# Kernel optimization log

Hardware: AMD Instinct MI355X
Metric: run time of the kernel (lower is better)

Reference implementation:

```python
import jax, jax.numpy as jnp
import numpy as np

N = 100000
E = 1600000
F_IN = 256   # 4 * 64 after concat
H = 128

def _glorot(key, shape):
    fan_in, fan_out = shape
    lim = jnp.sqrt(6.0 / (fan_in + fan_out))
    return jax.random.uniform(key, shape, jnp.float32, -lim, lim)

def setup_inputs() -> dict:
    key = jax.random.key(0)
    ks = jax.random.split(key, 32)
    inp = {
        'x': jax.random.normal(ks[0], (N, 64), jnp.float32),
        'diff': jax.random.normal(ks[1], (N, 64), jnp.float32),
        'rec_prev': jax.random.normal(ks[2], (N, 64), jnp.float32),
        'hidden_prev': jax.random.normal(ks[3], (N, 64), jnp.float32),
        'edge_index': jax.random.randint(ks[4], (2, E), 0, N, jnp.int64),
    }
    dims = [(F_IN, H), (H, H), (H, H), (H, 1)]
    for i, (din, dout) in enumerate(dims):
        inp[f'Wl{i}'] = _glorot(ks[5 + 3 * i], (din, dout))  # neighbor (aggr) weight
        inp[f'Wr{i}'] = _glorot(ks[6 + 3 * i], (din, dout))  # root weight
        inp[f'b{i}'] = jnp.zeros((dout,), jnp.float32)
    return inp

def _sage_conv(h, src, dst, Wl, Wr, b):
    # mean aggregation of source-node features at destination nodes (PyG SAGEConv)
    msg_sum = jax.ops.segment_sum(h[src], dst, num_segments=N)        # [N, F]
    cnt = jax.ops.segment_sum(jnp.ones((src.shape[0],), h.dtype), dst, num_segments=N)
    mean = msg_sum / jnp.maximum(cnt, 1.0)[:, None]
    return mean @ Wl + h @ Wr + b

def reference(x, diff, rec_prev, hidden_prev, edge_index,
              Wl0, Wr0, b0, Wl1, Wr1, b1, Wl2, Wr2, b2, Wl3, Wr3, b3):
    src, dst = edge_index[0], edge_index[1]
    h = jnp.concatenate([x, diff, rec_prev, hidden_prev], axis=1)  # [N, 256]
    params = [(Wl0, Wr0, b0), (Wl1, Wr1, b1), (Wl2, Wr2, b2), (Wl3, Wr3, b3)]
    h = _sage_conv(h, src, dst, *params[0])
    for Wl, Wr, b in params[1:]:
        h = jax.nn.relu(h)
        h = _sage_conv(h, src, dst, Wl, Wr, b)
    out = jax.nn.sigmoid(h)          # [N, 1]
    lwp_util = jnp.mean(out)
    return out, lwp_util
```

## Files before the change

### kernel.cpp

```cpp
#include <hip/hip_runtime.h>
#include <hip/hip_bf16.h>

#define NN 100000
#define EE 1600000
#define HH 128
#define NB 391
#define CAP 5120
#define GB 1563
#define SB 64
#define EPB (EE / SB)

typedef short bf16x8 __attribute__((ext_vector_type(8)));
typedef short bf16x4 __attribute__((ext_vector_type(4)));
typedef float f32x4  __attribute__((ext_vector_type(4)));

__device__ inline short f2bf(float v) {
    __hip_bfloat16 b = __float2bfloat16(v);
    return *reinterpret_cast<short*>(&b);
}

typedef __attribute__((address_space(1))) void gvoid_t;
typedef __attribute__((address_space(3))) void svoid_t;
__device__ __forceinline__ void gload16(const void* g, void* l) {
    __builtin_amdgcn_global_load_lds((gvoid_t*)g, (svoid_t*)l, 16, 0, 0);
}

__device__ __forceinline__ void ld_fence() { asm volatile("" ::: "memory"); }

template <int N>
__device__ __forceinline__ void wait_vm_bar() {
    if constexpr (N == 0)
        asm volatile("s_waitcnt vmcnt(0)\n\ts_barrier" ::: "memory");
    else if constexpr (N == 8)
        asm volatile("s_waitcnt vmcnt(8)\n\ts_barrier" ::: "memory");
    else if constexpr (N == 12)
        asm volatile("s_waitcnt vmcnt(12)\n\ts_barrier" ::: "memory");
    else if constexpr (N == 16)
        asm volatile("s_waitcnt vmcnt(16)\n\ts_barrier" ::: "memory");
    else if constexpr (N == 18)
        asm volatile("s_waitcnt vmcnt(18)\n\ts_barrier" ::: "memory");
    else if constexpr (N == 20)
        asm volatile("s_waitcnt vmcnt(20)\n\ts_barrier" ::: "memory");
    else
        static_assert(N == 0 || N == 8 || N == 12 || N == 16 || N == 18 || N == 20,
                      "bad N");
}
__device__ __forceinline__ void barrier_only() {
    asm volatile("s_barrier" ::: "memory");
}

__global__ __launch_bounds__(1024) void prep_kernel(
    const float* __restrict__ Wl0, const float* __restrict__ Wr0,
    const float* __restrict__ Wl1, const float* __restrict__ Wr1,
    const float* __restrict__ Wl2, const float* __restrict__ Wr2,
    __hip_bfloat16* __restrict__ WT0, __hip_bfloat16* __restrict__ WT1,
    __hip_bfloat16* __restrict__ WT2, int* __restrict__ bcur) {
    const int t = threadIdx.x;
    if (blockIdx.x == 128) {
        if (t < NB) bcur[t] = 0;
        return;
    }
    int id = blockIdx.x * 1024 + t;
    if (id < 65536) {
        int k = id & 255, n = id >> 8;
        float v = (n < 128) ? Wl0[(size_t)k * 128 + n]
                            : Wr0[(size_t)k * 128 + (n - 128)];
        WT0[(size_t)n * 256 + k] = __float2bfloat16(v);
    } else {
        id -= 65536;
        int layer = id >> 15;
        int u = id & 32767;
        int k = u & 127, n = u >> 7;
        const float* Wl = layer ? Wl2 : Wl1;
        const float* Wr = layer ? Wr2 : Wr1;
        __hip_bfloat16* WT = layer ? WT2 : WT1;
        float v = (n < 128) ? Wl[(size_t)k * 128 + n]
                            : Wr[(size_t)k * 128 + (n - 128)];
        WT[(size_t)n * 128 + k] = __float2bfloat16(v);
    }
}

#define EW 264
template <int K, bool FIRST>
__device__ __forceinline__ void gemm_body(
    short* __restrict__ lsh, int bid,
    const __hip_bfloat16* hin,
    const float* __restrict__ x0, const float* __restrict__ x1,
    const float* __restrict__ x2, const float* __restrict__ x3,
    const __hip_bfloat16* __restrict__ wt, const float* __restrict__ bias,
    __hip_bfloat16* zout, __hip_bfloat16* __restrict__ rout) {
    const int t    = threadIdx.x;
    const int w    = t >> 6;
    const int lane = t & 63;
    const int quad = lane >> 4;
    const int l16  = lane & 15;
    const int n0   = bid * 64;

    constexpr int BUFB = FIRST ? 16384 : 8192;
    char* const lc = (char*)lsh;

    const __hip_bfloat16* afeat[4];
#pragma unroll
    for (int ft = 0; ft < 4; ++ft)
        afeat[ft] = wt + (size_t)(w * 64 + ft * 16 + l16) * K + quad * 8;

    f32x4 acc[4][4];
#pragma unroll
    for (int ft = 0; ft < 4; ++ft)
#pragma unroll
        for (int nt = 0; nt < 4; ++nt)
            acc[ft][nt] = (f32x4){0.f, 0.f, 0.f, 0.f};

    bf16x8 wreg[2][8];

    auto loadW = [&](int p, int pb) {
#pragma unroll
        for (int kcl = 0; kcl < 2; ++kcl)
#pragma unroll
            for (int ft = 0; ft < 4; ++ft)
                wreg[pb][kcl * 4 + ft] =
                    *(const bf16x8*)(afeat[ft] + (p * 2 + kcl) * 32);
    };

    auto stage = [&](int p, int bb) {
        char* lb = lc + bb * BUFB;
        if constexpr (FIRST) {
            const float* sp = (p == 0) ? x0 : (p == 1) ? x1 : (p == 2) ? x2 : x3;
#pragma unroll
            for (int i = 0; i < 4; ++i) {
                const int j   = w * 4 + i;
                const int row = j * 4 + (lane >> 4);
                int rg = n0 + row; if (rg > NN - 1) rg = NN - 1;
                const int colb = ((lane & 15) * 16) ^ ((row & 15) << 4);
                gload16((const char*)sp + (size_t)rg * 256 + colb, lb + j * 1024);
            }
        } else {
#pragma unroll
            for (int i = 0; i < 2; ++i) {
                const int j   = w * 2 + i;
                const int row = j * 8 + (lane >> 3);
                int rg = n0 + row; if (rg > NN - 1) rg = NN - 1;
                const int colb = ((lane & 7) * 16) ^ ((row & 7) << 4);
                gload16((const char*)hin + (size_t)rg * 256 + p * 128 + colb,
                        lb + j * 1024);
            }
        }
    };

    auto compute = [&](int s, int bb, int pb) {
        const char* lb = lc + (bb)*BUFB;
#pragma unroll
        for (int kcl = 0; kcl < 2; ++kcl) {
#pragma unroll
            for (int nt = 0; nt < 4; ++nt) {
                const int row = nt * 16 + l16;
                bf16x8 b;
                if constexpr (FIRST) {
                    const int sw = (row & 15) << 4;
                    const int B0 = kcl * 128 + quad * 32;
                    const char* rb = lb + row * 256;
                    const f32x4 lo = *(const f32x4*)(rb + ((B0) ^ sw));
                    const f32x4 hi = *(const f32x4*)(rb + ((B0 + 16) ^ sw));
                    b[0] = f2bf(lo[0]); b[1] = f2bf(lo[1]);
                    b[2] = f2bf(lo[2]); b[3] = f2bf(lo[3]);
                    b[4] = f2bf(hi[0]); b[5] = f2bf(hi[1]);
                    b[6] = f2bf(hi[2]); b[7] = f2bf(hi[3]);
                } else {
                    const int sw = (row & 7) << 4;
                    const int B0 = kcl * 64 + quad * 16;
                    b = *(const bf16x8*)(lb + row * 128 + (B0 ^ sw));
                }
#pragma unroll
                for (int ft = 0; ft < 4; ++ft)
                    acc[ft][nt] = __builtin_amdgcn_mfma_f32_16x16x32_bf16(
                        wreg[pb][kcl * 4 + ft], b, acc[ft][nt], 0, 0, 0);
            }
        }
    };

    if constexpr (FIRST) {
        stage(0, 0); ld_fence();
        stage(1, 1); ld_fence();
        loadW(0, 0); ld_fence();
        wait_vm_bar<12>(); loadW(1, 1); stage(2, 2); compute(0, 0, 0); barrier_only();
        wait_vm_bar<20>(); loadW(2, 0); stage(3, 0); compute(1, 1, 1); barrier_only();
        wait_vm_bar<12>(); loadW(3, 1);              compute(2, 2, 0); barrier_only();
        wait_vm_bar<8>();                            compute(3, 0, 1); barrier_only();
    } else {
        stage(0, 0); ld_fence();
        stage(1, 1); ld_fence();
        loadW(0, 0); loadW(1, 1);
        wait_vm_bar<18>(); compute(0, 0, 0); barrier_only();
        wait_vm_bar<16>(); compute(1, 1, 1); barrier_only();
    }

#pragma unroll
    for (int ft = 0; ft < 4; ++ft) {
        const int fb = ft * 16 + quad * 4;
        float4 bv = make_float4(0.f, 0.f, 0.f, 0.f);
        if (w >= 2) bv = *(const float4*)&bias[(w - 2) * 64 + fb];
        const int cbase = (w & 1) * 64 + ((w >= 2) ? 128 : 0);
#pragma unroll
        for (int nt = 0; nt < 4; ++nt) {
            const f32x4 a = acc[ft][nt];
            bf16x4 p;
            p[0] = f2bf(a[0] + bv.x); p[1] = f2bf(a[1] + bv.y);
            p[2] = f2bf(a[2] + bv.z); p[3] = f2bf(a[3] + bv.w);
            *(bf16x4*)&lsh[(nt * 16 + l16) * EW + cbase + fb] = p;
        }
    }
    __syncthreads();
#pragma unroll
    for (int u = 0; u < 8; ++u) {
        const int id  = u * 256 + t;
        const int row = id >> 5, ch = (id & 31) * 8;
        const int nd  = n0 + row;
        if (nd < NN) {
            const bf16x8 v = *(const bf16x8*)&lsh[row * EW + ch];
            if (ch < 128) *(bf16x8*)&zout[(size_t)nd * HH + ch] = v;
            else          *(bf16x8*)&rout[(size_t)nd * HH + (ch - 128)] = v;
        }
    }
}

template <int K, bool FIRST>
__global__ __launch_bounds__(256) void gemm_kernel(
    const __hip_bfloat16* hin,
    const float* __restrict__ x0, const float* __restrict__ x1,
    const float* __restrict__ x2, const float* __restrict__ x3,
    const __hip_bfloat16* __restrict__ wt, const float* __restrict__ bias,
    __hip_bfloat16* zout, __hip_bfloat16* __restrict__ rout) {
    __shared__ short lsh[16896];
    gemm_body<K, FIRST>(lsh, blockIdx.x, hin, x0, x1, x2, x3, wt, bias, zout, rout);
}

__global__ __launch_bounds__(256) void gemm0_scatter_kernel(
    const float* __restrict__ x0, const float* __restrict__ x1,
    const float* __restrict__ x2, const float* __restrict__ x3,
    const __hip_bfloat16* __restrict__ wt, const float* __restrict__ bias,
    __hip_bfloat16* __restrict__ zout, __hip_bfloat16* __restrict__ rout,
    const int* __restrict__ srcv, const int* __restrict__ dstv,
    int* __restrict__ bcur, int* __restrict__ pairs) {
    __shared__ short lsh[24576];
    const int t = threadIdx.x;

    if (blockIdx.x >= SB) {
        gemm_body<256, true>(lsh, blockIdx.x - SB, nullptr, x0, x1, x2, x3,
                             wt, bias, zout, rout);
        return;
    }

    int* hist = (int*)lsh;
    int* base = hist + NB;
    for (int j = t; j < NB; j += 256) hist[j] = 0;
    __syncthreads();

    const int e0   = blockIdx.x * EPB;
    const int eend_ = e0 + EPB;

    for (int be = e0; be < eend_; be += 4096) {
        int d[16];
#pragma unroll
        for (int u = 0; u < 16; ++u) {
            const int e = be + u * 256 + t;
            d[u] = (e < eend_) ? dstv[e] : -1;
        }
#pragma unroll
        for (int u = 0; u < 16; ++u)
            if (d[u] >= 0) atomicAdd(&hist[d[u] >> 8], 1);
    }
    __syncthreads();

    for (int j = t; j < NB; j += 256)
        base[j] = hist[j] ? atomicAdd(&bcur[j], hist[j]) : 0;
    __syncthreads();
    for (int j = t; j < NB; j += 256) hist[j] = base[j];
    __syncthreads();

    for (int be = e0; be < eend_; be += 4096) {
        int s[16], d[16];
#pragma unroll
        for (int u = 0; u < 16; ++u) {
            const int e = be + u * 256 + t;
            if (e < eend_) { s[u] = srcv[e]; d[u] = dstv[e]; }
            else d[u] = -1;
        }
#pragma unroll
        for (int u = 0; u < 16; ++u)
            if (d[u] >= 0) {
                const int b   = d[u] >> 8;
                const int pos = atomicAdd(&hist[b], 1);
                if (pos < CAP) pairs[b * CAP + pos] = (s[u] << 8) | (d[u] & 255);
            }
    }
}

__global__ __launch_bounds__(256) void finalize_kernel(
    const int* __restrict__ bcur, const int* __restrict__ pairs,
    int* __restrict__ csr, int* __restrict__ beg, int* __restrict__ eend,
    float* __restrict__ inv) {
    __shared__ int cnt[256];
    __shared__ int scn[256];
    __shared__ int cur[256];
    const int b = blockIdx.x, t = threadIdx.x;
    int m = bcur[b];
    if (m > CAP) m = CAP;

    cnt[t] = 0;
    __syncthreads();
    for (int e = t; e < m; e += 256)
        atomicAdd(&cnt[pairs[b * CAP + e] & 255], 1);
    __syncthreads();

    const int v = cnt[t];
    scn[t] = v;
    __syncthreads();
    for (int st = 1; st < 256; st <<= 1) {
        int tv = (t >= st) ? scn[t - st] : 0;
        __syncthreads();
        scn[t] += tv;
        __syncthreads();
    }
    const int myStart = scn[t] - v;
    cur[t] = myStart;
    __syncthreads();

    for (int e = t; e < m; e += 256) {
        const int pk  = pairs[b * CAP + e];
        const int pos = atomicAdd(&cur[pk & 255], 1);
        csr[b * CAP + pos] = pk >> 8;
    }

    const int node = b * 256 + t;
    if (node < NN) {
        beg[node]  = b * CAP + myStart;
        eend[node] = b * CAP + myStart + v;
        inv[node]  = 1.0f / fmaxf((float)v, 1.0f);
    }
}

template <bool LAST>
__global__ __launch_bounds__(256) void aggregate_kernel(
    const __hip_bfloat16* __restrict__ z, __hip_bfloat16* __restrict__ rio,
    const int* __restrict__ beg, const int* __restrict__ eend,
    const int* __restrict__ csr, const float* __restrict__ inv,
    const float* __restrict__ Wl3, const float* __restrict__ Wr3,
    const float* __restrict__ b3, float* __restrict__ z3,
    float* __restrict__ r3) {
    const int i    = (blockIdx.x * 256 + threadIdx.x) >> 6;
    const int lane = threadIdx.x & 63;
    const int g    = lane >> 4;
    const int l16  = lane & 15;
    if (i >= NN) return;
    const int b0 = beg[i], e0 = eend[i];

    float acc[8];
#pragma unroll
    for (int j = 0; j < 8; ++j) acc[j] = 0.f;

    int e = b0 + g;
    for (; e + 12 < e0; e += 16) {
        const int s0 = csr[e];
        const int s1 = csr[e + 4];
        const int s2 = csr[e + 8];
        const int s3 = csr[e + 12];
        const bf16x8 z0 = *(const bf16x8*)&z[(size_t)s0 * HH + l16 * 8];
        const bf16x8 z1 = *(const bf16x8*)&z[(size_t)s1 * HH + l16 * 8];
        const bf16x8 z2 = *(const bf16x8*)&z[(size_t)s2 * HH + l16 * 8];
        const bf16x8 z3v = *(const bf16x8*)&z[(size_t)s3 * HH + l16 * 8];
        const __hip_bfloat162* p0 = (const __hip_bfloat162*)&z0;
        const __hip_bfloat162* p1 = (const __hip_bfloat162*)&z1;
        const __hip_bfloat162* p2 = (const __hip_bfloat162*)&z2;
        const __hip_bfloat162* p3 = (const __hip_bfloat162*)&z3v;
#pragma unroll
        for (int j = 0; j < 4; ++j) {
            acc[2 * j]     += __bfloat162float(p0[j].x) + __bfloat162float(p1[j].x)
                            + __bfloat162float(p2[j].x) + __bfloat162float(p3[j].x);
            acc[2 * j + 1] += __bfloat162float(p0[j].y) + __bfloat162float(p1[j].y)
                            + __bfloat162float(p2[j].y) + __bfloat162float(p3[j].y);
        }
    }
    for (; e < e0; e += 4) {
        const int s0 = csr[e];
        const bf16x8 z0 = *(const bf16x8*)&z[(size_t)s0 * HH + l16 * 8];
        const __hip_bfloat162* p0 = (const __hip_bfloat162*)&z0;
#pragma unroll
        for (int j = 0; j < 4; ++j) {
            acc[2 * j]     += __bfloat162float(p0[j].x);
            acc[2 * j + 1] += __bfloat162float(p0[j].y);
        }
    }

#pragma unroll
    for (int j = 0; j < 8; ++j) {
        acc[j] += __shfl_xor(acc[j], 16, 64);
        acc[j] += __shfl_xor(acc[j], 32, 64);
    }

    const float iv = inv[i];
    const int   f  = l16 * 8 + g * 2;
    const __hip_bfloat162 rv = *(const __hip_bfloat162*)&rio[(size_t)i * HH + f];
    const float ox = fmaxf(acc[g * 2]     * iv + __bfloat162float(rv.x), 0.f);
    const float oy = fmaxf(acc[g * 2 + 1] * iv + __bfloat162float(rv.y), 0.f);

    if (!LAST) {
        __hip_bfloat162 o;
        o.x = __float2bfloat16(ox);
        o.y = __float2bfloat16(oy);
        *(__hip_bfloat162*)&rio[(size_t)i * HH + f] = o;
    } else {
        const float2 wl = *(const float2*)&Wl3[f];
        const float2 wr = *(const float2*)&Wr3[f];
        float al = ox * wl.x + oy * wl.y;
        float ar = ox * wr.x + oy * wr.y;
#pragma unroll
        for (int m = 32; m; m >>= 1) {
            al += __shfl_xor(al, m, 64);
            ar += __shfl_xor(ar, m, 64);
        }
        if (lane == 0) {
            z3[i] = al;
            r3[i] = ar + b3[0];
        }
    }
}

__global__ __launch_bounds__(256) void final_kernel(
    const float* __restrict__ z3, const float* __restrict__ r3,
    const int* __restrict__ beg, const int* __restrict__ eend,
    const int* __restrict__ csr, const float* __restrict__ inv,
    float* __restrict__ out, float* __restrict__ partial) {
    __shared__ float red[4];
    const int i    = (blockIdx.x * 256 + threadIdx.x) >> 6;
    const int lane = threadIdx.x & 63;
    const int w    = threadIdx.x >> 6;
    float v = 0.f;
    if (i < NN) {
        const int b0 = beg[i], e0 = eend[i];
        float a = 0.f;
        for (int e = b0 + lane; e < e0; e += 64) a += z3[csr[e]];
#pragma unroll
        for (int m = 32; m; m >>= 1) a += __shfl_xor(a, m, 64);
        const float pre = a * inv[i] + r3[i];
        const float s = 1.f / (1.f + __expf(-pre));
        if (lane == 0) { out[i] = s; v = s; }
    }
    if (lane == 0) red[w] = v;
    __syncthreads();
    if (threadIdx.x == 0)
        partial[blockIdx.x] = red[0] + red[1] + red[2] + red[3];
}

__global__ __launch_bounds__(256) void mean_kernel(const float* __restrict__ partial,
                                                   int nb, float* __restrict__ out) {
    __shared__ float lds[256];
    float s = 0.f;
    for (int i = threadIdx.x; i < nb; i += 256) s += partial[i];
    lds[threadIdx.x] = s;
    __syncthreads();
    for (int st = 128; st; st >>= 1) {
        if (threadIdx.x < st) lds[threadIdx.x] += lds[threadIdx.x + st];
        __syncthreads();
    }
    if (threadIdx.x == 0) out[NN] = lds[0] / (float)NN;
}

extern "C" void kernel_launch(void* const* d_in, const int* in_sizes, int n_in,
                              void* d_out, int out_size, void* d_ws, size_t ws_size,
                              hipStream_t stream) {
    const float* x    = (const float*)d_in[0];
    const float* diff = (const float*)d_in[1];
    const float* rec  = (const float*)d_in[2];
    const float* hid  = (const float*)d_in[3];
    const int* edge   = (const int*)d_in[4];
    const int* esrc = edge;
    const int* edst = edge + EE;
    const float* Wl0 = (const float*)d_in[5];
    const float* Wr0 = (const float*)d_in[6];
    const float* b0  = (const float*)d_in[7];
    const float* Wl1 = (const float*)d_in[8];
    const float* Wr1 = (const float*)d_in[9];
    const float* b1  = (const float*)d_in[10];
    const float* Wl2 = (const float*)d_in[11];
    const float* Wr2 = (const float*)d_in[12];
    const float* b2  = (const float*)d_in[13];
    const float* Wl3 = (const float*)d_in[14];
    const float* Wr3 = (const float*)d_in[15];
    const float* b3  = (const float*)d_in[16];
    float* out = (float*)d_out;

    char* w = (char*)d_ws;
    auto alloc = [&](size_t bytes) -> void* {
        void* p = (void*)w;
        w += (bytes + 255) & ~(size_t)255;
        return p;
    };
    __hip_bfloat16* bufA = (__hip_bfloat16*)alloc((size_t)NN * HH * 2);
    __hip_bfloat16* bufB = (__hip_bfloat16*)alloc((size_t)NN * HH * 2);
    __hip_bfloat16* WT0  = (__hip_bfloat16*)alloc((size_t)256 * 256 * 2);
    __hip_bfloat16* WT1  = (__hip_bfloat16*)alloc((size_t)256 * 128 * 2);
    __hip_bfloat16* WT2  = (__hip_bfloat16*)alloc((size_t)256 * 128 * 2);
    int*   pairs   = (int*)alloc((size_t)NB * CAP * 4);
    int*   csr     = (int*)alloc((size_t)NB * CAP * 4);
    int*   bcur    = (int*)alloc((size_t)512 * 4);
    int*   beg     = (int*)alloc((size_t)NN * 4);
    int*   eend    = (int*)alloc((size_t)NN * 4);
    float* inv     = (float*)alloc((size_t)NN * 4);
    float* z3      = (float*)alloc((size_t)NN * 4);
    float* r3      = (float*)alloc((size_t)NN * 4);
    float* partial = (float*)alloc((size_t)25000 * 4);

    const int WB = (NN + 3) / 4;

    prep_kernel<<<129, 1024, 0, stream>>>(Wl0, Wr0, Wl1, Wr1, Wl2, Wr2,
                                          WT0, WT1, WT2, bcur);

    gemm0_scatter_kernel<<<GB + SB, 256, 0, stream>>>(
        x, diff, rec, hid, WT0, b0, bufA, bufB, esrc, edst, bcur, pairs);

    finalize_kernel<<<NB, 256, 0, stream>>>(bcur, pairs, csr, beg, eend, inv);

    aggregate_kernel<false><<<WB, 256, 0, stream>>>(bufA, bufB, beg, eend, csr, inv,
                                                    nullptr, nullptr, nullptr,
                                                    nullptr, nullptr);

    gemm_kernel<128, false><<<GB, 256, 0, stream>>>(bufB, nullptr, nullptr, nullptr, nullptr,
                                                    WT1, b1, bufB, bufA);
    aggregate_kernel<false><<<WB, 256, 0, stream>>>(bufB, bufA, beg, eend, csr, inv,
                                                    nullptr, nullptr, nullptr,
                                                    nullptr, nullptr);

    gemm_kernel<128, false><<<GB, 256, 0, stream>>>(bufA, nullptr, nullptr, nullptr, nullptr,
                                                    WT2, b2, bufA, bufB);
    aggregate_kernel<true><<<WB, 256, 0, stream>>>(bufA, bufB, beg, eend, csr, inv,
                                                   Wl3, Wr3, b3, z3, r3);

    final_kernel<<<WB, 256, 0, stream>>>(z3, r3, beg, eend, csr, inv, out, partial);
    mean_kernel<<<1, 256, 0, stream>>>(partial, WB, out);
}
```

Measured before the change: 497.7 us.

## Split fused gemm0/scatter kernel and issue all GEMM tile loads upfront

Separates the combined first-layer GEMM plus edge-scatter kernel into a standalone scatter kernel (now 256 blocks instead of 64) and a dedicated gemm0 kernel. The GEMM body no longer double-buffers: it loads all weight fragments and stages all K-slices into LDS at once (larger LDS, 64KB for the first layer), then waits on decreasing vmcnt thresholds and computes each slice as it arrives. The aim is more memory parallelism per block and more scatter parallelism. The cost is an extra kernel launch and the loss of concurrent scatter/GEMM overlap. Higher register and LDS use may also lower occupancy.

```diff
diff --git a/kernel.cpp b/kernel.cpp
--- a/kernel.cpp
+++ b/kernel.cpp
@@ -7,7 +7,7 @@
 #define NB 391
 #define CAP 5120
 #define GB 1563
-#define SB 64
+#define SB 256
 #define EPB (EE / SB)
 
 typedef short bf16x8 __attribute__((ext_vector_type(8)));
@@ -31,19 +31,16 @@
 __device__ __forceinline__ void wait_vm_bar() {
     if constexpr (N == 0)
         asm volatile("s_waitcnt vmcnt(0)\n\ts_barrier" ::: "memory");
+    else if constexpr (N == 2)
+        asm volatile("s_waitcnt vmcnt(2)\n\ts_barrier" ::: "memory");
+    else if constexpr (N == 4)
+        asm volatile("s_waitcnt vmcnt(4)\n\ts_barrier" ::: "memory");
     else if constexpr (N == 8)
         asm volatile("s_waitcnt vmcnt(8)\n\ts_barrier" ::: "memory");
     else if constexpr (N == 12)
         asm volatile("s_waitcnt vmcnt(12)\n\ts_barrier" ::: "memory");
-    else if constexpr (N == 16)
-        asm volatile("s_waitcnt vmcnt(16)\n\ts_barrier" ::: "memory");
-    else if constexpr (N == 18)
-        asm volatile("s_waitcnt vmcnt(18)\n\ts_barrier" ::: "memory");
-    else if constexpr (N == 20)
-        asm volatile("s_waitcnt vmcnt(20)\n\ts_barrier" ::: "memory");
     else
-        static_assert(N == 0 || N == 8 || N == 12 || N == 16 || N == 18 || N == 20,
-                      "bad N");
+        static_assert(N == 0 || N == 2 || N == 4 || N == 8 || N == 12, "bad N");
 }
 __device__ __forceinline__ void barrier_only() {
     asm volatile("s_barrier" ::: "memory");
@@ -96,6 +93,7 @@
     const int l16  = lane & 15;
     const int n0   = bid * 64;
 
+    constexpr int NS   = K / 64;
     constexpr int BUFB = FIRST ? 16384 : 8192;
     char* const lc = (char*)lsh;
 
@@ -111,19 +109,19 @@
         for (int nt = 0; nt < 4; ++nt)
             acc[ft][nt] = (f32x4){0.f, 0.f, 0.f, 0.f};
 
-    bf16x8 wreg[2][8];
-
-    auto loadW = [&](int p, int pb) {
+    bf16x8 wreg[NS][8];
+
+    auto loadW = [&](int p) {
 #pragma unroll
         for (int kcl = 0; kcl < 2; ++kcl)
 #pragma unroll
             for (int ft = 0; ft < 4; ++ft)
-                wreg[pb][kcl * 4 + ft] =
+                wreg[p][kcl * 4 + ft] =
                     *(const bf16x8*)(afeat[ft] + (p * 2 + kcl) * 32);
     };
 
-    auto stage = [&](int p, int bb) {
-        char* lb = lc + bb * BUFB;
+    auto stage = [&](int p) {
+        char* lb = lc + p * BUFB;
         if constexpr (FIRST) {
             const float* sp = (p == 0) ? x0 : (p == 1) ? x1 : (p == 2) ? x2 : x3;
 #pragma unroll
@@ -147,8 +145,8 @@
         }
     };
 
-    auto compute = [&](int s, int bb, int pb) {
-        const char* lb = lc + (bb)*BUFB;
+    auto compute = [&](int s) {
+        const char* lb = lc + s * BUFB;
 #pragma unroll
         for (int kcl = 0; kcl < 2; ++kcl) {
 #pragma unroll
@@ -173,25 +171,29 @@
 #pragma unroll
                 for (int ft = 0; ft < 4; ++ft)
                     acc[ft][nt] = __builtin_amdgcn_mfma_f32_16x16x32_bf16(
-                        wreg[pb][kcl * 4 + ft], b, acc[ft][nt], 0, 0, 0);
+                        wreg[s][kcl * 4 + ft], b, acc[ft][nt], 0, 0, 0);
             }
         }
     };
 
     if constexpr (FIRST) {
-        stage(0, 0); ld_fence();
-        stage(1, 1); ld_fence();
-        loadW(0, 0); ld_fence();
-        wait_vm_bar<12>(); loadW(1, 1); stage(2, 2); compute(0, 0, 0); barrier_only();
-        wait_vm_bar<20>(); loadW(2, 0); stage(3, 0); compute(1, 1, 1); barrier_only();
-        wait_vm_bar<12>(); loadW(3, 1);              compute(2, 2, 0); barrier_only();
-        wait_vm_bar<8>();                            compute(3, 0, 1); barrier_only();
+        loadW(0); loadW(1); loadW(2); loadW(3); ld_fence();
+        stage(0); ld_fence();
+        stage(1); ld_fence();
+        stage(2); ld_fence();
+        stage(3); ld_fence();
+        wait_vm_bar<12>(); compute(0);
+        wait_vm_bar<8>();  compute(1);
+        wait_vm_bar<4>();  compute(2);
+        wait_vm_bar<0>();  compute(3);
+        barrier_only();
     } else {
-        stage(0, 0); ld_fence();
-        stage(1, 1); ld_fence();
-        loadW(0, 0); loadW(1, 1);
-        wait_vm_bar<18>(); compute(0, 0, 0); barrier_only();
-        wait_vm_bar<16>(); compute(1, 1, 1); barrier_only();
+        loadW(0); loadW(1); ld_fence();
+        stage(0); ld_fence();
+        stage(1); ld_fence();
+        wait_vm_bar<2>(); compute(0);
+        wait_vm_bar<0>(); compute(1);
+        barrier_only();
     }
 
 #pragma unroll
@@ -223,39 +225,37 @@
     }
 }
 
-template <int K, bool FIRST>
-__global__ __launch_bounds__(256) void gemm_kernel(
-    const __hip_bfloat16* hin,
+__global__ __launch_bounds__(256, 2) void gemm0_kernel(
     const float* __restrict__ x0, const float* __restrict__ x1,
     const float* __restrict__ x2, const float* __restrict__ x3,
     const __hip_bfloat16* __restrict__ wt, const float* __restrict__ bias,
+    __hip_bfloat16* __restrict__ zout, __hip_bfloat16* __restrict__ rout) {
+    __shared__ short lsh[32768];
+    gemm_body<256, true>(lsh, blockIdx.x, nullptr, x0, x1, x2, x3,
+                         wt, bias, zout, rout);
+}
+
+template <int K>
+__global__ __launch_bounds__(256) void gemm_kernel(
+    const __hip_bfloat16* hin,
+    const __hip_bfloat16* __restrict__ wt, const float* __restrict__ bias,
     __hip_bfloat16* zout, __hip_bfloat16* __restrict__ rout) {
     __shared__ short lsh[16896];
-    gemm_body<K, FIRST>(lsh, blockIdx.x, hin, x0, x1, x2, x3, wt, bias, zout, rout);
-}
-
-__global__ __launch_bounds__(256) void gemm0_scatter_kernel(
-    const float* __restrict__ x0, const float* __restrict__ x1,
-    const float* __restrict__ x2, const float* __restrict__ x3,
-    const __hip_bfloat16* __restrict__ wt, const float* __restrict__ bias,
-    __hip_bfloat16* __restrict__ zout, __hip_bfloat16* __restrict__ rout,
+    gemm_body<K, false>(lsh, blockIdx.x, hin, nullptr, nullptr, nullptr, nullptr,
+                        wt, bias, zout, rout);
+}
+
+__global__ __launch_bounds__(256) void scatter_kernel(
     const int* __restrict__ srcv, const int* __restrict__ dstv,
     int* __restrict__ bcur, int* __restrict__ pairs) {
-    __shared__ short lsh[24576];
+    __shared__ int hist[NB];
+    __shared__ int base[NB];
     const int t = threadIdx.x;
 
-    if (blockIdx.x >= SB) {
-        gemm_body<256, true>(lsh, blockIdx.x - SB, nullptr, x0, x1, x2, x3,
-                             wt, bias, zout, rout);
-        return;
-    }
-
-    int* hist = (int*)lsh;
-    int* base = hist + NB;
     for (int j = t; j < NB; j += 256) hist[j] = 0;
     __syncthreads();
 
-    const int e0   = blockIdx.x * EPB;
+    const int e0    = blockIdx.x * EPB;
     const int eend_ = e0 + EPB;
 
     for (int be = e0; be < eend_; be += 4096) {
@@ -515,8 +515,9 @@
     prep_kernel<<<129, 1024, 0, stream>>>(Wl0, Wr0, Wl1, Wr1, Wl2, Wr2,
                                           WT0, WT1, WT2, bcur);
 
-    gemm0_scatter_kernel<<<GB + SB, 256, 0, stream>>>(
-        x, diff, rec, hid, WT0, b0, bufA, bufB, esrc, edst, bcur, pairs);
+    scatter_kernel<<<SB, 256, 0, stream>>>(esrc, edst, bcur, pairs);
+
+    gemm0_kernel<<<GB, 256, 0, stream>>>(x, diff, rec, hid, WT0, b0, bufA, bufB);
 
     finalize_kernel<<<NB, 256, 0, stream>>>(bcur, pairs, csr, beg, eend, inv);
 
@@ -524,14 +525,12 @@
                                                     nullptr, nullptr, nullptr,
                                                     nullptr, nullptr);
 
-    gemm_kernel<128, false><<<GB, 256, 0, stream>>>(bufB, nullptr, nullptr, nullptr, nullptr,
-                                                    WT1, b1, bufB, bufA);
+    gemm_kernel<128><<<GB, 256, 0, stream>>>(bufB, WT1, b1, bufB, bufA);
     aggregate_kernel<false><<<WB, 256, 0, stream>>>(bufB, bufA, beg, eend, csr, inv,
                                                     nullptr, nullptr, nullptr,
                                                     nullptr, nullptr);
 
-    gemm_kernel<128, false><<<GB, 256, 0, stream>>>(bufA, nullptr, nullptr, nullptr, nullptr,
-                                                    WT2, b2, bufA, bufB);
+    gemm_kernel<128><<<GB, 256, 0, stream>>>(bufA, WT2, b2, bufA, bufB);
     aggregate_kernel<true><<<WB, 256, 0, stream>>>(bufA, bufB, beg, eend, csr, inv,
                                                    Wl3, Wr3, b3, z3, r3);
 
```

Result: slower. 512.4 us (+3.0%).

## Move layer-0 GEMM to run alongside CSR finalize and widen edge scatter

Applied to the files above, without the earlier changes.

The first-layer GEMM is now co-scheduled with the CSR finalize kernel instead of the edge scatter, and the scatter runs as its own launch with 256 blocks instead of 64. The final kernel maps four nodes per wavefront using 16-lane groups, so low-degree nodes no longer leave most lanes idle. This is meant to raise parallelism in the scatter pass and cut wasted lanes in the last reduction, at the cost of more atomics on the global bucket counters and a different overlap pattern.

```diff
diff --git a/kernel.cpp b/kernel.cpp
--- a/kernel.cpp
+++ b/kernel.cpp
@@ -7,8 +7,9 @@
 #define NB 391
 #define CAP 5120
 #define GB 1563
-#define SB 64
+#define SB 256
 #define EPB (EE / SB)
+#define FB 6250
 
 typedef short bf16x8 __attribute__((ext_vector_type(8)));
 typedef short bf16x4 __attribute__((ext_vector_type(4)));
@@ -148,7 +149,7 @@
     };
 
     auto compute = [&](int s, int bb, int pb) {
-        const char* lb = lc + (bb)*BUFB;
+        const char* lb = lc + bb * BUFB;
 #pragma unroll
         for (int kcl = 0; kcl < 2; ++kcl) {
 #pragma unroll
@@ -223,39 +224,27 @@
     }
 }
 
-template <int K, bool FIRST>
+template <int K>
 __global__ __launch_bounds__(256) void gemm_kernel(
     const __hip_bfloat16* hin,
-    const float* __restrict__ x0, const float* __restrict__ x1,
-    const float* __restrict__ x2, const float* __restrict__ x3,
     const __hip_bfloat16* __restrict__ wt, const float* __restrict__ bias,
     __hip_bfloat16* zout, __hip_bfloat16* __restrict__ rout) {
     __shared__ short lsh[16896];
-    gemm_body<K, FIRST>(lsh, blockIdx.x, hin, x0, x1, x2, x3, wt, bias, zout, rout);
-}
-
-__global__ __launch_bounds__(256) void gemm0_scatter_kernel(
-    const float* __restrict__ x0, const float* __restrict__ x1,
-    const float* __restrict__ x2, const float* __restrict__ x3,
-    const __hip_bfloat16* __restrict__ wt, const float* __restrict__ bias,
-    __hip_bfloat16* __restrict__ zout, __hip_bfloat16* __restrict__ rout,
+    gemm_body<K, false>(lsh, blockIdx.x, hin, nullptr, nullptr, nullptr, nullptr,
+                        wt, bias, zout, rout);
+}
+
+__global__ __launch_bounds__(256) void scatter_kernel(
     const int* __restrict__ srcv, const int* __restrict__ dstv,
     int* __restrict__ bcur, int* __restrict__ pairs) {
-    __shared__ short lsh[24576];
+    __shared__ int hist[NB];
+    __shared__ int base[NB];
     const int t = threadIdx.x;
 
-    if (blockIdx.x >= SB) {
-        gemm_body<256, true>(lsh, blockIdx.x - SB, nullptr, x0, x1, x2, x3,
-                             wt, bias, zout, rout);
-        return;
-    }
-
-    int* hist = (int*)lsh;
-    int* base = hist + NB;
     for (int j = t; j < NB; j += 256) hist[j] = 0;
     __syncthreads();
 
-    const int e0   = blockIdx.x * EPB;
+    const int e0    = blockIdx.x * EPB;
     const int eend_ = e0 + EPB;
 
     for (int be = e0; be < eend_; be += 4096) {
@@ -295,14 +284,27 @@
     }
 }
 
-__global__ __launch_bounds__(256) void finalize_kernel(
+__global__ __launch_bounds__(256) void fin_gemm0_kernel(
+    const float* __restrict__ x0, const float* __restrict__ x1,
+    const float* __restrict__ x2, const float* __restrict__ x3,
+    const __hip_bfloat16* __restrict__ wt, const float* __restrict__ bias,
+    __hip_bfloat16* __restrict__ zout, __hip_bfloat16* __restrict__ rout,
     const int* __restrict__ bcur, const int* __restrict__ pairs,
     int* __restrict__ csr, int* __restrict__ beg, int* __restrict__ eend,
     float* __restrict__ inv) {
-    __shared__ int cnt[256];
-    __shared__ int scn[256];
-    __shared__ int cur[256];
-    const int b = blockIdx.x, t = threadIdx.x;
+    __shared__ short lsh[24576];
+    const int t = threadIdx.x;
+
+    if (blockIdx.x >= NB) {
+        gemm_body<256, true>(lsh, blockIdx.x - NB, nullptr, x0, x1, x2, x3,
+                             wt, bias, zout, rout);
+        return;
+    }
+
+    int* cnt = (int*)lsh;
+    int* scn = cnt + 256;
+    int* cur = scn + 256;
+    const int b = blockIdx.x;
     int m = bcur[b];
     if (m > CAP) m = CAP;
 
@@ -431,21 +433,28 @@
     const int* __restrict__ csr, const float* __restrict__ inv,
     float* __restrict__ out, float* __restrict__ partial) {
     __shared__ float red[4];
-    const int i    = (blockIdx.x * 256 + threadIdx.x) >> 6;
+    const int wv   = (blockIdx.x * 256 + threadIdx.x) >> 6;
     const int lane = threadIdx.x & 63;
+    const int sub  = lane >> 4;
+    const int l16  = lane & 15;
     const int w    = threadIdx.x >> 6;
-    float v = 0.f;
+    const int i    = wv * 4 + sub;
+    float s = 0.f;
     if (i < NN) {
         const int b0 = beg[i], e0 = eend[i];
         float a = 0.f;
-        for (int e = b0 + lane; e < e0; e += 64) a += z3[csr[e]];
-#pragma unroll
-        for (int m = 32; m; m >>= 1) a += __shfl_xor(a, m, 64);
+        for (int e = b0 + l16; e < e0; e += 16) a += z3[csr[e]];
+        a += __shfl_xor(a, 1, 64);
+        a += __shfl_xor(a, 2, 64);
+        a += __shfl_xor(a, 4, 64);
+        a += __shfl_xor(a, 8, 64);
         const float pre = a * inv[i] + r3[i];
-        const float s = 1.f / (1.f + __expf(-pre));
-        if (lane == 0) { out[i] = s; v = s; }
-    }
-    if (lane == 0) red[w] = v;
+        const float sg  = 1.f / (1.f + __expf(-pre));
+        if (l16 == 0) { out[i] = sg; s = sg; }
+    }
+    s += __shfl_xor(s, 16, 64);
+    s += __shfl_xor(s, 32, 64);
+    if (lane == 0) red[w] = s;
     __syncthreads();
     if (threadIdx.x == 0)
         partial[blockIdx.x] = red[0] + red[1] + red[2] + red[3];
@@ -515,26 +524,25 @@
     prep_kernel<<<129, 1024, 0, stream>>>(Wl0, Wr0, Wl1, Wr1, Wl2, Wr2,
                                           WT0, WT1, WT2, bcur);
 
-    gemm0_scatter_kernel<<<GB + SB, 256, 0, stream>>>(
-        x, diff, rec, hid, WT0, b0, bufA, bufB, esrc, edst, bcur, pairs);
-
-    finalize_kernel<<<NB, 256, 0, stream>>>(bcur, pairs, csr, beg, eend, inv);
+    scatter_kernel<<<SB, 256, 0, stream>>>(esrc, edst, bcur, pairs);
+
+    fin_gemm0_kernel<<<NB + GB, 256, 0, stream>>>(
+        x, diff, rec, hid, WT0, b0, bufA, bufB,
+        bcur, pairs, csr, beg, eend, inv);
 
     aggregate_kernel<false><<<WB, 256, 0, stream>>>(bufA, bufB, beg, eend, csr, inv,
                                                     nullptr, nullptr, nullptr,
                                                     nullptr, nullptr);
 
-    gemm_kernel<128, false><<<GB, 256, 0, stream>>>(bufB, nullptr, nullptr, nullptr, nullptr,
-                                                    WT1, b1, bufB, bufA);
+    gemm_kernel<128><<<GB, 256, 0, stream>>>(bufB, WT1, b1, bufB, bufA);
     aggregate_kernel<false><<<WB, 256, 0, stream>>>(bufB, bufA, beg, eend, csr, inv,
                                                     nullptr, nullptr, nullptr,
                                                     nullptr, nullptr);
 
-    gemm_kernel<128, false><<<GB, 256, 0, stream>>>(bufA, nullptr, nullptr, nullptr, nullptr,
-                                                    WT2, b2, bufA, bufB);
+    gemm_kernel<128><<<GB, 256, 0, stream>>>(bufA, WT2, b2, bufA, bufB);
     aggregate_kernel<true><<<WB, 256, 0, stream>>>(bufA, bufB, beg, eend, csr, inv,
                                                    Wl3, Wr3, b3, z3, r3);
 
-    final_kernel<<<WB, 256, 0, stream>>>(z3, r3, beg, eend, csr, inv, out, partial);
-    mean_kernel<<<1, 256, 0, stream>>>(partial, WB, out);
-}
+    final_kernel<<<FB, 256, 0, stream>>>(z3, r3, beg, eend, csr, inv, out, partial);
+    mean_kernel<<<1, 256, 0, stream>>>(partial, FB, out);
+}
```

Result: faster. 468.1 us (-5.9%).
